# Performance work log

Hardware: AMD Instinct MI355X
Metric: run time of the kernel (lower is better)

The kernel has to match this reference:

```python
import jax, jax.numpy as jnp
import numpy as np

B, IN, H = 4096, 1024, 2048

def setup_inputs() -> dict:
    key = jax.random.key(0)
    ks = jax.random.split(key, 7)
    sk = (1.0 / H) ** 0.5
    return {
        "x": jax.random.normal(ks[0], (B, IN), dtype=jnp.float32),
        "prev_h": jax.random.normal(ks[1], (B, H), dtype=jnp.float32),
        "prev_c": jax.random.normal(ks[2], (B, H), dtype=jnp.float32),
        "W_i": jax.random.uniform(ks[3], (H, H + IN), dtype=jnp.float32, minval=-sk, maxval=sk),
        "W_f": jax.random.uniform(ks[4], (H, H + IN), dtype=jnp.float32, minval=-sk, maxval=sk),
        "W_o": jax.random.uniform(ks[5], (H, H + IN), dtype=jnp.float32, minval=-sk, maxval=sk),
        "W_c": jax.random.uniform(ks[6], (H, H + IN), dtype=jnp.float32, minval=-sk, maxval=sk),
    }

def reference(x, prev_h, prev_c, W_i, W_f, W_o, W_c):
    # concat (h, x) along features: [B, H+IN]
    hx = jnp.concatenate([prev_h, x], axis=1)
    # stack 4 gate weights -> single GEMM: [B, H+IN] @ [H+IN, 4H]
    W = jnp.concatenate([W_i, W_f, W_o, W_c], axis=0)  # [4H, H+IN]
    gates = hx @ W.T  # [B, 4H]
    gi, gf, go, gc = jnp.split(gates, 4, axis=1)
    i = jax.nn.sigmoid(gi)
    f = jax.nn.sigmoid(gf)
    o = jax.nn.sigmoid(go)
    c_tilde = jnp.tanh(gc)
    next_c = f * prev_c + i * c_tilde
    next_h = o * jnp.tanh(next_c)
    return next_h, next_c
```

## Files before the change

kernel.cpp:

```cpp
#include <hip/hip_runtime.h>
#include <hip/hip_bf16.h>


#define BATCH 4096
#define INW   1024
#define HID   2048
#define GK    3072
#define GN    8192

typedef __attribute__((ext_vector_type(8))) short short8;
typedef __attribute__((ext_vector_type(4))) float floatx4;

__device__ __forceinline__ unsigned short f2bf(float f) {
    union { float f; unsigned u; } v; v.f = f;
    unsigned r = v.u + 0x7FFFu + ((v.u >> 16) & 1u);
    return (unsigned short)(r >> 16);
}
__device__ __forceinline__ float bf2f(unsigned short u) {
    union { unsigned u; float f; } v; v.u = ((unsigned)u) << 16;
    return v.f;
}
__device__ __forceinline__ float sigf(float x) {
    return 1.0f / (1.0f + __expf(-x));
}
__device__ __forceinline__ float tanhfast(float x) {
    float t = __expf(fminf(fmaxf(2.0f * x, -30.0f), 30.0f));
    return (t - 1.0f) / (t + 1.0f);
}

__global__ __launch_bounds__(256) void cvt_bf16(const float4* __restrict__ src,
                                                unsigned short* __restrict__ dst,
                                                int src_w4, int dst_stride, int n4) {
    int i = blockIdx.x * 256 + threadIdx.x;
    if (i >= n4) return;
    int row = i / src_w4;
    int c4  = i - row * src_w4;
    float4 v = src[i];
    ushort4 o;
    o.x = f2bf(v.x); o.y = f2bf(v.y); o.z = f2bf(v.z); o.w = f2bf(v.w);
    *(ushort4*)&dst[(size_t)row * dst_stride + (size_t)c4 * 4] = o;
}

__device__ __forceinline__ void gld16(const unsigned short* g, unsigned short* l) {
    __builtin_amdgcn_global_load_lds((const __attribute__((address_space(1))) unsigned int*)g,
                                     (__attribute__((address_space(3))) unsigned int*)l,
                                     16, 0, 0);
}

__global__ __launch_bounds__(256) void gemm_bt(const unsigned short* __restrict__ A,
                                               const unsigned short* __restrict__ Bt,
                                               unsigned short* __restrict__ C) {
    __shared__ unsigned short lA[128 * 32];
    __shared__ unsigned short lB[128 * 32];
    const int tid  = threadIdx.x;
    const int wave = tid >> 6;
    const int lane = tid & 63;
    const long row0 = (long)blockIdx.x * 128;
    const long col0 = (long)blockIdx.y * 128;

    const int sr = tid >> 2;
    const int sk = (tid & 3) << 3;
    const unsigned short* gA0 = A  + (row0 + sr)      * GK + sk;
    const unsigned short* gA1 = A  + (row0 + 64 + sr) * GK + sk;
    const unsigned short* gB0 = Bt + (col0 + sr)      * GK + sk;
    const unsigned short* gB1 = Bt + (col0 + 64 + sr) * GK + sk;
    unsigned short* lA0 = &lA[wave * 512];
    unsigned short* lA1 = &lA[2048 + wave * 512];
    unsigned short* lB0 = &lB[wave * 512];
    unsigned short* lB1 = &lB[2048 + wave * 512];

    floatx4 acc[4][4];
    #pragma unroll
    for (int mi = 0; mi < 4; mi++)
        #pragma unroll
        for (int ni = 0; ni < 4; ni++)
            acc[mi][ni] = (floatx4)(0.0f);

    const int mBase = (wave >> 1) << 6;
    const int nBase = (wave & 1) << 6;
    const int fr = lane & 15;
    const int kq = (lane >> 4) << 3;

    for (int k0 = 0; k0 < GK; k0 += 32) {
        __syncthreads();
        gld16(gA0 + k0, lA0);
        gld16(gA1 + k0, lA1);
        gld16(gB0 + k0, lB0);
        gld16(gB1 + k0, lB1);
        __syncthreads();

        short8 af[4], bfv[4];
        #pragma unroll
        for (int mi = 0; mi < 4; mi++)
            af[mi] = *(const short8*)&lA[(mBase + mi * 16 + fr) * 32 + kq];
        #pragma unroll
        for (int ni = 0; ni < 4; ni++)
            bfv[ni] = *(const short8*)&lB[(nBase + ni * 16 + fr) * 32 + kq];
        #pragma unroll
        for (int mi = 0; mi < 4; mi++)
            #pragma unroll
            for (int ni = 0; ni < 4; ni++)
                acc[mi][ni] = __builtin_amdgcn_mfma_f32_16x16x32_bf16(af[mi], bfv[ni], acc[mi][ni], 0, 0, 0);
    }

    const int cr = (lane >> 4) << 2;
    const int cc = lane & 15;
    #pragma unroll
    for (int mi = 0; mi < 4; mi++) {
        #pragma unroll
        for (int ni = 0; ni < 4; ni++) {
            long base = (row0 + mBase + mi * 16 + cr) * (long)GN + col0 + nBase + ni * 16 + cc;
            #pragma unroll
            for (int r = 0; r < 4; r++)
                C[base + (long)r * GN] = f2bf(acc[mi][ni][r]);
        }
    }
}

__global__ __launch_bounds__(256) void lstm_ep(const unsigned short* __restrict__ gates,
                                               const float* __restrict__ prev_c,
                                               float* __restrict__ out) {
    const int i = blockIdx.x * 256 + threadIdx.x;
    const int b = i >> 9;
    const int h = (i & 511) << 2;
    const size_t gb = (size_t)b * GN + h;
    ushort4 gi = *(const ushort4*)&gates[gb];
    ushort4 gf = *(const ushort4*)&gates[gb + HID];
    ushort4 go = *(const ushort4*)&gates[gb + 2 * HID];
    ushort4 gc = *(const ushort4*)&gates[gb + 3 * HID];
    const size_t ob = (size_t)b * HID + h;
    float4 c4 = *(const float4*)&prev_c[ob];

    unsigned short giv[4] = {gi.x, gi.y, gi.z, gi.w};
    unsigned short gfv[4] = {gf.x, gf.y, gf.z, gf.w};
    unsigned short gov[4] = {go.x, go.y, go.z, go.w};
    unsigned short gcv[4] = {gc.x, gc.y, gc.z, gc.w};
    float cv[4] = {c4.x, c4.y, c4.z, c4.w};
    float nh[4], nc[4];
    #pragma unroll
    for (int j = 0; j < 4; j++) {
        float vi = sigf(bf2f(giv[j]));
        float vf = sigf(bf2f(gfv[j]));
        float vo = sigf(bf2f(gov[j]));
        float vc = tanhfast(bf2f(gcv[j]));
        float ncf = vf * cv[j] + vi * vc;
        float nhf = vo * tanhfast(ncf);
        nc[j] = ncf;
        nh[j] = nhf;
    }
    float4 vh = {nh[0], nh[1], nh[2], nh[3]};
    float4 vc4 = {nc[0], nc[1], nc[2], nc[3]};
    *(float4*)&out[ob] = vh;
    *(float4*)&out[(size_t)BATCH * HID + ob] = vc4;
}

extern "C" void kernel_launch(void* const* d_in, const int* in_sizes, int n_in,
                              void* d_out, int out_size, void* d_ws, size_t ws_size,
                              hipStream_t stream) {
    const float* x   = (const float*)d_in[0];
    const float* ph  = (const float*)d_in[1];
    const float* pc  = (const float*)d_in[2];
    const float* Wi  = (const float*)d_in[3];
    const float* Wf  = (const float*)d_in[4];
    const float* Wo  = (const float*)d_in[5];
    const float* Wc  = (const float*)d_in[6];

    unsigned short* hx    = (unsigned short*)d_ws;
    unsigned short* Wb    = hx + (size_t)BATCH * GK;
    unsigned short* gates = Wb + (size_t)GN * GK;
    float* out = (float*)d_out;

    cvt_bf16<<<8192, 256, 0, stream>>>((const float4*)ph, hx,       HID / 4, GK, BATCH * (HID / 4));
    cvt_bf16<<<4096, 256, 0, stream>>>((const float4*)x,  hx + HID, INW / 4, GK, BATCH * (INW / 4));
    cvt_bf16<<<6144, 256, 0, stream>>>((const float4*)Wi, Wb,                        GK / 4, GK, HID * (GK / 4));
    cvt_bf16<<<6144, 256, 0, stream>>>((const float4*)Wf, Wb + (size_t)HID * GK,     GK / 4, GK, HID * (GK / 4));
    cvt_bf16<<<6144, 256, 0, stream>>>((const float4*)Wo, Wb + (size_t)2 * HID * GK, GK / 4, GK, HID * (GK / 4));
    cvt_bf16<<<6144, 256, 0, stream>>>((const float4*)Wc, Wb + (size_t)3 * HID * GK, GK / 4, GK, HID * (GK / 4));

    gemm_bt<<<dim3(BATCH / 128, GN / 128), 256, 0, stream>>>(hx, Wb, gates);

    lstm_ep<<<(BATCH * HID / 4) / 256, 256, 0, stream>>>(gates, pc, out);
}
```

Before: 467.6 us.

## Fuse LSTM epilogue into GEMM with gate-interleaved weights and single pack kernel

The weight rows are interleaved per hidden unit (i,f,o,c adjacent), so each GEMM output tile holds all four gates for a group of hidden units. The LSTM pointwise math then runs in the GEMM epilogue through an LDS staging buffer, which removes the bf16 gates round-trip to global memory and the separate epilogue kernel. The six conversion launches are merged into one pack kernel. The cost is a heavier epilogue with scalar, less coalesced loads of prev_c and stores of the outputs.

```diff
diff --git a/kernel.cpp b/kernel.cpp
--- a/kernel.cpp
+++ b/kernel.cpp
@@ -16,10 +16,6 @@
     unsigned r = v.u + 0x7FFFu + ((v.u >> 16) & 1u);
     return (unsigned short)(r >> 16);
 }
-__device__ __forceinline__ float bf2f(unsigned short u) {
-    union { unsigned u; float f; } v; v.u = ((unsigned)u) << 16;
-    return v.f;
-}
 __device__ __forceinline__ float sigf(float x) {
     return 1.0f / (1.0f + __expf(-x));
 }
@@ -28,17 +24,41 @@
     return (t - 1.0f) / (t + 1.0f);
 }
 
-__global__ __launch_bounds__(256) void cvt_bf16(const float4* __restrict__ src,
-                                                unsigned short* __restrict__ dst,
-                                                int src_w4, int dst_stride, int n4) {
-    int i = blockIdx.x * 256 + threadIdx.x;
-    if (i >= n4) return;
-    int row = i / src_w4;
-    int c4  = i - row * src_w4;
-    float4 v = src[i];
+__global__ __launch_bounds__(256) void pack_all(const float4* __restrict__ ph,
+                                                const float4* __restrict__ x,
+                                                const float4* __restrict__ Wi,
+                                                const float4* __restrict__ Wf,
+                                                const float4* __restrict__ Wo,
+                                                const float4* __restrict__ Wc,
+                                                unsigned short* __restrict__ hx,
+                                                unsigned short* __restrict__ Wb) {
+    long i = (long)blockIdx.x * 256 + threadIdx.x;
+    float4 v;
+    unsigned short* dst;
+    if (i < 2097152L) {
+        int r  = (int)(i >> 9);
+        int c4 = (int)(i & 511);
+        v = ph[i];
+        dst = hx + (size_t)r * GK + (size_t)c4 * 4;
+    } else if (i < 3145728L) {
+        long j = i - 2097152L;
+        int r  = (int)(j >> 8);
+        int c4 = (int)(j & 255);
+        v = x[j];
+        dst = hx + (size_t)r * GK + HID + (size_t)c4 * 4;
+    } else {
+        long j = i - 3145728L;
+        int g  = (int)(j / 1572864L);
+        long jj = j - (long)g * 1572864L;
+        int r  = (int)(jj / 768);
+        int c4 = (int)(jj - (long)r * 768);
+        const float4* Wg = (g == 0) ? Wi : (g == 1) ? Wf : (g == 2) ? Wo : Wc;
+        v = Wg[jj];
+        dst = Wb + ((size_t)r * 4 + g) * GK + (size_t)c4 * 4;
+    }
     ushort4 o;
     o.x = f2bf(v.x); o.y = f2bf(v.y); o.z = f2bf(v.z); o.w = f2bf(v.w);
-    *(ushort4*)&dst[(size_t)row * dst_stride + (size_t)c4 * 4] = o;
+    *(ushort4*)dst = o;
 }
 
 __device__ __forceinline__ void gld16(const unsigned short* g, unsigned short* l) {
@@ -47,11 +67,13 @@
                                      16, 0, 0);
 }
 
-__global__ __launch_bounds__(256) void gemm_bt(const unsigned short* __restrict__ A,
-                                               const unsigned short* __restrict__ Bt,
-                                               unsigned short* __restrict__ C) {
-    __shared__ unsigned short lA[128 * 32];
-    __shared__ unsigned short lB[128 * 32];
+__global__ __launch_bounds__(256) void gemm_lstm(const unsigned short* __restrict__ A,
+                                                 const unsigned short* __restrict__ Bt,
+                                                 const float* __restrict__ pc,
+                                                 float* __restrict__ out) {
+    __shared__ __attribute__((aligned(16))) unsigned short smem[128 * 32 * 2];
+    unsigned short* lA = smem;
+    unsigned short* lB = smem + 128 * 32;
     const int tid  = threadIdx.x;
     const int wave = tid >> 6;
     const int lane = tid & 63;
@@ -103,55 +125,38 @@
                 acc[mi][ni] = __builtin_amdgcn_mfma_f32_16x16x32_bf16(af[mi], bfv[ni], acc[mi][ni], 0, 0, 0);
     }
 
+    __syncthreads();
+    float* epi = (float*)smem + wave * 1024;
     const int cr = (lane >> 4) << 2;
     const int cc = lane & 15;
+    const long hh_base = (col0 + nBase) >> 2;
+
     #pragma unroll
     for (int mi = 0; mi < 4; mi++) {
         #pragma unroll
-        for (int ni = 0; ni < 4; ni++) {
-            long base = (row0 + mBase + mi * 16 + cr) * (long)GN + col0 + nBase + ni * 16 + cc;
+        for (int ni = 0; ni < 4; ni++)
             #pragma unroll
             for (int r = 0; r < 4; r++)
-                C[base + (long)r * GN] = f2bf(acc[mi][ni][r]);
+                epi[(cr + r) * 64 + cc + 16 * ni] = acc[mi][ni][r];
+        #pragma unroll
+        for (int it = 0; it < 4; it++) {
+            int idx = it * 64 + lane;
+            int rl = idx >> 4;
+            int hl = idx & 15;
+            float4 g4 = *(const float4*)&epi[rl * 64 + hl * 4];
+            long rg = row0 + mBase + mi * 16 + rl;
+            long hg = hh_base + hl;
+            float pcv = pc[rg * HID + hg];
+            float vi = sigf(g4.x);
+            float vf = sigf(g4.y);
+            float vo = sigf(g4.z);
+            float ct = tanhfast(g4.w);
+            float ncf = vf * pcv + vi * ct;
+            float nhf = vo * tanhfast(ncf);
+            out[rg * HID + hg] = nhf;
+            out[(size_t)BATCH * HID + rg * HID + hg] = ncf;
         }
     }
-}
-
-__global__ __launch_bounds__(256) void lstm_ep(const unsigned short* __restrict__ gates,
-                                               const float* __restrict__ prev_c,
-                                               float* __restrict__ out) {
-    const int i = blockIdx.x * 256 + threadIdx.x;
-    const int b = i >> 9;
-    const int h = (i & 511) << 2;
-    const size_t gb = (size_t)b * GN + h;
-    ushort4 gi = *(const ushort4*)&gates[gb];
-    ushort4 gf = *(const ushort4*)&gates[gb + HID];
-    ushort4 go = *(const ushort4*)&gates[gb + 2 * HID];
-    ushort4 gc = *(const ushort4*)&gates[gb + 3 * HID];
-    const size_t ob = (size_t)b * HID + h;
-    float4 c4 = *(const float4*)&prev_c[ob];
-
-    unsigned short giv[4] = {gi.x, gi.y, gi.z, gi.w};
-    unsigned short gfv[4] = {gf.x, gf.y, gf.z, gf.w};
-    unsigned short gov[4] = {go.x, go.y, go.z, go.w};
-    unsigned short gcv[4] = {gc.x, gc.y, gc.z, gc.w};
-    float cv[4] = {c4.x, c4.y, c4.z, c4.w};
-    float nh[4], nc[4];
-    #pragma unroll
-    for (int j = 0; j < 4; j++) {
-        float vi = sigf(bf2f(giv[j]));
-        float vf = sigf(bf2f(gfv[j]));
-        float vo = sigf(bf2f(gov[j]));
-        float vc = tanhfast(bf2f(gcv[j]));
-        float ncf = vf * cv[j] + vi * vc;
-        float nhf = vo * tanhfast(ncf);
-        nc[j] = ncf;
-        nh[j] = nhf;
-    }
-    float4 vh = {nh[0], nh[1], nh[2], nh[3]};
-    float4 vc4 = {nc[0], nc[1], nc[2], nc[3]};
-    *(float4*)&out[ob] = vh;
-    *(float4*)&out[(size_t)BATCH * HID + ob] = vc4;
 }
 
 extern "C" void kernel_launch(void* const* d_in, const int* in_sizes, int n_in,
@@ -165,19 +170,14 @@
     const float* Wo  = (const float*)d_in[5];
     const float* Wc  = (const float*)d_in[6];
 
-    unsigned short* hx    = (unsigned short*)d_ws;
-    unsigned short* Wb    = hx + (size_t)BATCH * GK;
-    unsigned short* gates = Wb + (size_t)GN * GK;
+    unsigned short* hx = (unsigned short*)d_ws;
+    unsigned short* Wb = hx + (size_t)BATCH * GK;
     float* out = (float*)d_out;
 
-    cvt_bf16<<<8192, 256, 0, stream>>>((const float4*)ph, hx,       HID / 4, GK, BATCH * (HID / 4));
-    cvt_bf16<<<4096, 256, 0, stream>>>((const float4*)x,  hx + HID, INW / 4, GK, BATCH * (INW / 4));
-    cvt_bf16<<<6144, 256, 0, stream>>>((const float4*)Wi, Wb,                        GK / 4, GK, HID * (GK / 4));
-    cvt_bf16<<<6144, 256, 0, stream>>>((const float4*)Wf, Wb + (size_t)HID * GK,     GK / 4, GK, HID * (GK / 4));
-    cvt_bf16<<<6144, 256, 0, stream>>>((const float4*)Wo, Wb + (size_t)2 * HID * GK, GK / 4, GK, HID * (GK / 4));
-    cvt_bf16<<<6144, 256, 0, stream>>>((const float4*)Wc, Wb + (size_t)3 * HID * GK, GK / 4, GK, HID * (GK / 4));
+    pack_all<<<36864, 256, 0, stream>>>((const float4*)ph, (const float4*)x,
+                                        (const float4*)Wi, (const float4*)Wf,
+                                        (const float4*)Wo, (const float4*)Wc,
+                                        hx, Wb);
 
-    gemm_bt<<<dim3(BATCH / 128, GN / 128), 256, 0, stream>>>(hx, Wb, gates);
-
-    lstm_ep<<<(BATCH * HID / 4) / 256, 256, 0, stream>>>(gates, pc, out);
+    gemm_lstm<<<dim3(BATCH / 128, GN / 128), 256, 0, stream>>>(hx, Wb, pc, out);
 }
```

Result: slower. 504.6 us (+7.9%).
